# Optimization experiments

Hardware: AMD Instinct MI355X
Metric: run time of the kernel (lower is better)

Reference implementation:

```python
import jax, jax.numpy as jnp
import numpy as np

HUGE = 1e9  # stand-in for ops.HUGE_INT


def setup_inputs() -> dict:
    key = jax.random.key(0)
    ks = jax.random.split(key, 8)
    B, Q, K = 8, 128, 256
    Dq = Dk = Dv = H = 512
    query = jax.random.normal(ks[0], (B, Q, Dq), dtype=jnp.float32)
    k_ = jax.random.normal(ks[1], (B, K, Dk), dtype=jnp.float32)
    value = jax.random.normal(ks[2], (B, K, Dv), dtype=jnp.float32)
    mask = jax.random.randint(ks[3], (B, K), 0, 2, dtype=jnp.int32)
    # FFN params: linear1 (Dq+Dk -> H, bias), linear2 (H -> 1, no bias)
    W1 = jax.random.normal(ks[4], (Dq + Dk, H), dtype=jnp.float32) * 0.05
    b1 = jax.random.normal(ks[5], (H,), dtype=jnp.float32) * 0.05
    w2 = jax.random.normal(ks[6], (H, 1), dtype=jnp.float32) * 0.05
    return {"query": query, "key": k_, "value": value, "mask": mask,
            "W1": W1, "b1": b1, "w2": w2}


def reference(query, key, value, mask, W1, b1, w2):
    # Additive (FFN) attention. Original tiles query/key into [B, Q*K, Dq+Dk]
    # and applies linear1; concat@W1 is separable, so we project q and k
    # separately and broadcast-add (same math, no tiled concat tensor).
    Dq = query.shape[-1]
    Wq, Wk = W1[:Dq], W1[Dq:]
    q_proj = jnp.einsum('bqd,dh->bqh', query, Wq)   # [B,Q,H]
    k_proj = jnp.einsum('bkd,dh->bkh', key, Wk)     # [B,K,H]
    hidden = jnp.tanh(q_proj[:, :, None, :] + k_proj[:, None, :, :] + b1)  # [B,Q,K,H]
    scores = jnp.einsum('bqkh,h->bqk', hidden, w2[:, 0])  # [B,Q,K]
    # padding mask fill BEFORE scaling, matching the original op order
    scores = jnp.where(mask[:, None, :] != 0, -HUGE, scores)
    scores = scores / jnp.sqrt(jnp.float32(key.shape[-1]))
    attn_weights = jax.nn.softmax(scores, axis=-1)
    attn_vec = jnp.einsum('bqk,bkv->bqv', attn_weights, value)  # dropout=0 at eval
    return attn_vec, attn_weights
```

## Files before the change

### kernel.cpp

```cpp
#include <hip/hip_runtime.h>
#include <hip/hip_bf16.h>

#define B_ 8
#define Q_ 128
#define K_ 256
#define D_ 512
#define TWOLOG2E 2.8853900817779268f
#define SCALE 0.044194173824159216f
#define L2E 1.4426950408889634f
#define MASKVAL (-44194173.824159216f)

typedef __attribute__((ext_vector_type(8))) short frag8;
typedef __attribute__((ext_vector_type(4))) float f32x4;

__device__ __forceinline__ float fexp2(float x) {
  float r;
  asm("v_exp_f32 %0, %1" : "=v"(r) : "v"(x));
  return r;
}
__device__ __forceinline__ float frcp(float x) {
  float r;
  asm("v_rcp_f32 %0, %1" : "=v"(r) : "v"(x));
  return r;
}
__device__ __forceinline__ unsigned f2bf_u(float x) {
  unsigned u = __float_as_uint(x);
  return (u + 0x7FFFu + ((u >> 16) & 1u)) >> 16;
}
__device__ __forceinline__ unsigned short f2bf(float x) {
  return (unsigned short)f2bf_u(x);
}
__device__ __forceinline__ unsigned packbf(float lo, float hi) {
  return f2bf_u(lo) | (f2bf_u(hi) << 16);
}

__global__ __launch_bounds__(256) void gemm_kernel(
    const float* __restrict__ query, const float* __restrict__ key,
    const float* __restrict__ W1, const float* __restrict__ b1,
    float* __restrict__ qp, float* __restrict__ kpbT) {
  __shared__ short As[32 * 64];
  __shared__ short Bs[64 * 72];
  const int t = threadIdx.x;
  const int m0 = blockIdx.y * 32;
  const int n0 = blockIdx.x * 64;
  const bool is_k = (m0 >= B_ * Q_);
  const float* X = is_k ? key : query;
  const int xrow0 = is_k ? (m0 - B_ * Q_) : m0;
  const float* Wb = W1 + (is_k ? (size_t)D_ * D_ : 0);

  const int am = t >> 3;
  const int ac = t & 7;
  const float* gA = X + (size_t)(xrow0 + am) * D_ + ac * 8;
  short* aw = As + am * 64 + ((ac ^ (am & 7)) * 8);

  const int prow = t >> 4;
  const int n4 = (t & 15) * 4;
  const float* gB = Wb + n0 + n4;

  const int l = t & 63;
  const int w = t >> 6;
  const int lr = l & 15;
  const int kg = l >> 4;
  const int key8 = lr & 7;
  int aoff[2][2], boff[2];
#pragma unroll
  for (int kk = 0; kk < 2; ++kk) {
    const int cposA = ((kg + kk * 4) ^ key8) * 8;
#pragma unroll
    for (int mt = 0; mt < 2; ++mt) aoff[mt][kk] = (mt * 16 + lr) * 64 + cposA;
    boff[kk] = (w * 16 + lr) * 72 + (kg + kk * 4) * 8;
  }

  f32x4 acc[2];
  acc[0] = (f32x4){0.f, 0.f, 0.f, 0.f};
  acc[1] = (f32x4){0.f, 0.f, 0.f, 0.f};

  for (int k0 = 0; k0 < D_; k0 += 64) {
    float4 a0 = *(const float4*)(gA + k0);
    float4 a1 = *(const float4*)(gA + k0 + 4);
    float4 w00 = *(const float4*)(gB + (size_t)(k0 + 2 * prow) * D_);
    float4 w01 = *(const float4*)(gB + (size_t)(k0 + 2 * prow + 1) * D_);
    float4 w10 = *(const float4*)(gB + (size_t)(k0 + 2 * prow + 32) * D_);
    float4 w11 = *(const float4*)(gB + (size_t)(k0 + 2 * prow + 33) * D_);
    __syncthreads();
    {
      union { frag8 f; unsigned short u[8]; } av;
      av.u[0] = f2bf(a0.x); av.u[1] = f2bf(a0.y); av.u[2] = f2bf(a0.z); av.u[3] = f2bf(a0.w);
      av.u[4] = f2bf(a1.x); av.u[5] = f2bf(a1.y); av.u[6] = f2bf(a1.z); av.u[7] = f2bf(a1.w);
      *(frag8*)aw = av.f;
    }
    {
      float lo0[4] = {w00.x, w00.y, w00.z, w00.w};
      float hi0[4] = {w01.x, w01.y, w01.z, w01.w};
      float lo1[4] = {w10.x, w10.y, w10.z, w10.w};
      float hi1[4] = {w11.x, w11.y, w11.z, w11.w};
#pragma unroll
      for (int j = 0; j < 4; ++j) {
        *(unsigned*)(Bs + (n4 + j) * 72 + 2 * prow) = packbf(lo0[j], hi0[j]);
        *(unsigned*)(Bs + (n4 + j) * 72 + 2 * (prow + 16)) = packbf(lo1[j], hi1[j]);
      }
    }
    __syncthreads();
#pragma unroll
    for (int kk = 0; kk < 2; ++kk) {
      frag8 bf = *(const frag8*)(Bs + boff[kk]);
#pragma unroll
      for (int mt = 0; mt < 2; ++mt) {
        frag8 af = *(const frag8*)(As + aoff[mt][kk]);
        acc[mt] = __builtin_amdgcn_mfma_f32_16x16x32_bf16(af, bf, acc[mt], 0, 0, 0);
      }
    }
  }

  const int col = n0 + w * 16 + lr;
  if (is_k) {
    const float bc = b1[col];
#pragma unroll
    for (int mt = 0; mt < 2; ++mt) {
      const int krow = m0 - B_ * Q_ + mt * 16 + kg * 4;
      const int bb = krow >> 8;
      const int kk0 = krow & 255;
      float4 v;
      v.x = fexp2((acc[mt][0] + bc) * TWOLOG2E);
      v.y = fexp2((acc[mt][1] + bc) * TWOLOG2E);
      v.z = fexp2((acc[mt][2] + bc) * TWOLOG2E);
      v.w = fexp2((acc[mt][3] + bc) * TWOLOG2E);
      *(float4*)&kpbT[((size_t)bb * D_ + col) * K_ + kk0] = v;
    }
  } else {
#pragma unroll
    for (int mt = 0; mt < 2; ++mt) {
#pragma unroll
      for (int i = 0; i < 4; ++i) {
        const int row = m0 + mt * 16 + kg * 4 + i;
        qp[(size_t)row * D_ + col] = fexp2(acc[mt][i] * TWOLOG2E);
      }
    }
  }
}

__global__ __launch_bounds__(1024) void score_kernel(
    const float* __restrict__ qp, const float* __restrict__ kpbT,
    const int* __restrict__ mask, const float* __restrict__ w2,
    float* __restrict__ out_w) {
  __shared__ float smem_p[16 * 512];
  const int b = blockIdx.y;
  const int q0 = blockIdx.x * 4;
  const int t = threadIdx.x;
  const int lane = t & 63;
  const int w = __builtin_amdgcn_readfirstlane(t >> 6);
  const int kc = w & 1;
  const int hq = w >> 1;
  const int h0 = hq * 64;

  {
    const float* pk = kpbT + ((size_t)b * D_ + h0) * K_ + kc * 128 + 2 * lane;
    const float* q_0 = qp + (size_t)(b * Q_ + q0 + 0) * D_ + h0;
    const float* q_1 = qp + (size_t)(b * Q_ + q0 + 1) * D_ + h0;
    const float* q_2 = qp + (size_t)(b * Q_ + q0 + 2) * D_ + h0;
    const float* q_3 = qp + (size_t)(b * Q_ + q0 + 3) * D_ + h0;
    const float* w2h = w2 + h0;

    float2 a0 = {0.f, 0.f}, a1 = {0.f, 0.f}, a2 = {0.f, 0.f}, a3 = {0.f, 0.f};
    for (int h = 0; h < 64; h += 8) {
      float2 kv[8];
#pragma unroll
      for (int j = 0; j < 8; ++j) kv[j] = *(const float2*)&pk[(size_t)(h + j) * K_];
      float4 e0a = *(const float4*)(q_0 + h), e0b = *(const float4*)(q_0 + h + 4);
      float4 e1a = *(const float4*)(q_1 + h), e1b = *(const float4*)(q_1 + h + 4);
      float4 e2a = *(const float4*)(q_2 + h), e2b = *(const float4*)(q_2 + h + 4);
      float4 e3a = *(const float4*)(q_3 + h), e3b = *(const float4*)(q_3 + h + 4);
      float4 wa = *(const float4*)(w2h + h), wb = *(const float4*)(w2h + h + 4);
      float E0[8] = {e0a.x, e0a.y, e0a.z, e0a.w, e0b.x, e0b.y, e0b.z, e0b.w};
      float E1[8] = {e1a.x, e1a.y, e1a.z, e1a.w, e1b.x, e1b.y, e1b.z, e1b.w};
      float E2[8] = {e2a.x, e2a.y, e2a.z, e2a.w, e2b.x, e2b.y, e2b.z, e2b.w};
      float E3[8] = {e3a.x, e3a.y, e3a.z, e3a.w, e3b.x, e3b.y, e3b.z, e3b.w};
      float WV[8] = {wa.x, wa.y, wa.z, wa.w, wb.x, wb.y, wb.z, wb.w};
#pragma unroll
      for (int j = 0; j < 8; ++j) {
        a0.x = fmaf(WV[j], frcp(fmaf(E0[j], kv[j].x, 1.f)), a0.x);
        a0.y = fmaf(WV[j], frcp(fmaf(E0[j], kv[j].y, 1.f)), a0.y);
        a1.x = fmaf(WV[j], frcp(fmaf(E1[j], kv[j].x, 1.f)), a1.x);
        a1.y = fmaf(WV[j], frcp(fmaf(E1[j], kv[j].y, 1.f)), a1.y);
        a2.x = fmaf(WV[j], frcp(fmaf(E2[j], kv[j].x, 1.f)), a2.x);
        a2.y = fmaf(WV[j], frcp(fmaf(E2[j], kv[j].y, 1.f)), a2.y);
        a3.x = fmaf(WV[j], frcp(fmaf(E3[j], kv[j].x, 1.f)), a3.x);
        a3.y = fmaf(WV[j], frcp(fmaf(E3[j], kv[j].y, 1.f)), a3.y);
      }
    }
    *(float2*)&smem_p[w * 512 + 0 * 128 + 2 * lane] = a0;
    *(float2*)&smem_p[w * 512 + 1 * 128 + 2 * lane] = a1;
    *(float2*)&smem_p[w * 512 + 2 * 128 + 2 * lane] = a2;
    *(float2*)&smem_p[w * 512 + 3 * 128 + 2 * lane] = a3;
  }
  __syncthreads();

  if (w < 4) {
    const int q = w;
    float sw = 0.f;
#pragma unroll
    for (int m = 0; m < 8; ++m) sw += w2[lane + 64 * m];
#pragma unroll
    for (int off = 32; off; off >>= 1) sw += __shfl_xor(sw, off);

    float s[4];
#pragma unroll
    for (int r = 0; r < 4; ++r) {
      const int kcc = r >> 1;
      const int off = (r & 1) * 64 + lane;
      float p = 0.f;
#pragma unroll
      for (int hh = 0; hh < 8; ++hh)
        p += smem_p[(hh * 2 + kcc) * 512 + q * 128 + off];
      const int mk = mask[b * K_ + r * 64 + lane];
      s[r] = mk ? MASKVAL : fmaf(-2.f, p, sw) * SCALE;
    }
    float mx = fmaxf(fmaxf(s[0], s[1]), fmaxf(s[2], s[3]));
#pragma unroll
    for (int off = 32; off; off >>= 1) mx = fmaxf(mx, __shfl_xor(mx, off));
    float e[4], sum = 0.f;
#pragma unroll
    for (int r = 0; r < 4; ++r) {
      e[r] = fexp2((s[r] - mx) * L2E);
      sum += e[r];
    }
#pragma unroll
    for (int off = 32; off; off >>= 1) sum += __shfl_xor(sum, off);
    const float inv = frcp(sum);
    float* ow = out_w + (size_t)(b * Q_ + q0 + q) * K_;
#pragma unroll
    for (int r = 0; r < 4; ++r) ow[r * 64 + lane] = e[r] * inv;
  }
}

__global__ __launch_bounds__(1024) void pv_kernel(
    const float* __restrict__ out_w, const float* __restrict__ value,
    float* __restrict__ out_vec) {
  const int b = blockIdx.y;
  const int qt = blockIdx.x >> 3;
  const int ct = blockIdx.x & 7;
  const int t = threadIdx.x;
  const int lane = t & 63;
  const int w = __builtin_amdgcn_readfirstlane(t >> 6);
  const int col = ct * 64 + lane;
  const int q0 = qt * 32 + w * 2;

  const float* pw0 = out_w + (size_t)(b * Q_ + q0) * K_;
  const float* pw1 = pw0 + K_;
  const float* vb = value + (size_t)b * K_ * D_ + col;

  float o0 = 0.f, o1 = 0.f;
  for (int k = 0; k < K_; k += 4) {
    const float4 p0 = *(const float4*)&pw0[k];
    const float4 p1 = *(const float4*)&pw1[k];
    const float v0 = vb[(size_t)(k + 0) * D_];
    const float v1 = vb[(size_t)(k + 1) * D_];
    const float v2 = vb[(size_t)(k + 2) * D_];
    const float v3 = vb[(size_t)(k + 3) * D_];
    o0 = fmaf(p0.x, v0, fmaf(p0.y, v1, fmaf(p0.z, v2, fmaf(p0.w, v3, o0))));
    o1 = fmaf(p1.x, v0, fmaf(p1.y, v1, fmaf(p1.z, v2, fmaf(p1.w, v3, o1))));
  }
  out_vec[(size_t)(b * Q_ + q0) * D_ + col] = o0;
  out_vec[(size_t)(b * Q_ + q0 + 1) * D_ + col] = o1;
}

extern "C" void kernel_launch(void* const* d_in, const int* in_sizes, int n_in,
                              void* d_out, int out_size, void* d_ws, size_t ws_size,
                              hipStream_t stream) {
  const float* query = (const float*)d_in[0];
  const float* key   = (const float*)d_in[1];
  const float* value = (const float*)d_in[2];
  const int*   mask  = (const int*)d_in[3];
  const float* W1    = (const float*)d_in[4];
  const float* b1    = (const float*)d_in[5];
  const float* w2    = (const float*)d_in[6];

  float* out_vec = (float*)d_out;
  float* out_w   = out_vec + (size_t)B_ * Q_ * D_;

  float* qp   = (float*)d_ws;
  float* kpbT = qp + (size_t)B_ * Q_ * D_;

  gemm_kernel<<<dim3(8, 96), 256, 0, stream>>>(query, key, W1, b1, qp, kpbT);
  score_kernel<<<dim3(Q_ / 4, B_), 1024, 0, stream>>>(qp, kpbT, mask, w2, out_w);
  pv_kernel<<<dim3(32, B_), 1024, 0, stream>>>(out_w, value, out_vec);
}
```

Before: 113.9 us.

## Split score kernel over key halves and move softmax into PV kernel

The score kernel now splits each query tile's keys across two blocks, doubling the grid, and has each wave reduce 32 hidden units instead of 64. It writes raw masked scores to a workspace buffer. The softmax moves into the PV kernel, which normalises 32 rows into shared memory before the weighted sum over values. Softmax is recomputed by all 8 column blocks, and an extra score buffer adds a global round trip.

```diff
diff --git a/kernel.cpp b/kernel.cpp
--- a/kernel.cpp
+++ b/kernel.cpp
@@ -142,19 +142,19 @@
 __global__ __launch_bounds__(1024) void score_kernel(
     const float* __restrict__ qp, const float* __restrict__ kpbT,
     const int* __restrict__ mask, const float* __restrict__ w2,
-    float* __restrict__ out_w) {
+    float* __restrict__ sc) {
   __shared__ float smem_p[16 * 512];
   const int b = blockIdx.y;
-  const int q0 = blockIdx.x * 4;
+  const int qt = blockIdx.x >> 1;
+  const int kh = blockIdx.x & 1;
+  const int q0 = qt * 4;
   const int t = threadIdx.x;
   const int lane = t & 63;
   const int w = __builtin_amdgcn_readfirstlane(t >> 6);
-  const int kc = w & 1;
-  const int hq = w >> 1;
-  const int h0 = hq * 64;
+  const int h0 = w * 32;
 
   {
-    const float* pk = kpbT + ((size_t)b * D_ + h0) * K_ + kc * 128 + 2 * lane;
+    const float* pk = kpbT + ((size_t)b * D_ + h0) * K_ + kh * 128 + 2 * lane;
     const float* q_0 = qp + (size_t)(b * Q_ + q0 + 0) * D_ + h0;
     const float* q_1 = qp + (size_t)(b * Q_ + q0 + 1) * D_ + h0;
     const float* q_2 = qp + (size_t)(b * Q_ + q0 + 2) * D_ + h0;
@@ -162,7 +162,7 @@
     const float* w2h = w2 + h0;
 
     float2 a0 = {0.f, 0.f}, a1 = {0.f, 0.f}, a2 = {0.f, 0.f}, a3 = {0.f, 0.f};
-    for (int h = 0; h < 64; h += 8) {
+    for (int h = 0; h < 32; h += 8) {
       float2 kv[8];
 #pragma unroll
       for (int j = 0; j < 8; ++j) kv[j] = *(const float2*)&pk[(size_t)(h + j) * K_];
@@ -203,50 +203,58 @@
 #pragma unroll
     for (int off = 32; off; off >>= 1) sw += __shfl_xor(sw, off);
 
-    float s[4];
-#pragma unroll
-    for (int r = 0; r < 4; ++r) {
-      const int kcc = r >> 1;
-      const int off = (r & 1) * 64 + lane;
+    float* srow = sc + (size_t)(b * Q_ + q0 + q) * K_ + kh * 128;
+#pragma unroll
+    for (int half = 0; half < 2; ++half) {
+      const int pos = half * 64 + lane;
       float p = 0.f;
 #pragma unroll
-      for (int hh = 0; hh < 8; ++hh)
-        p += smem_p[(hh * 2 + kcc) * 512 + q * 128 + off];
-      const int mk = mask[b * K_ + r * 64 + lane];
-      s[r] = mk ? MASKVAL : fmaf(-2.f, p, sw) * SCALE;
-    }
-    float mx = fmaxf(fmaxf(s[0], s[1]), fmaxf(s[2], s[3]));
-#pragma unroll
-    for (int off = 32; off; off >>= 1) mx = fmaxf(mx, __shfl_xor(mx, off));
-    float e[4], sum = 0.f;
-#pragma unroll
-    for (int r = 0; r < 4; ++r) {
-      e[r] = fexp2((s[r] - mx) * L2E);
-      sum += e[r];
-    }
-#pragma unroll
-    for (int off = 32; off; off >>= 1) sum += __shfl_xor(sum, off);
-    const float inv = frcp(sum);
-    float* ow = out_w + (size_t)(b * Q_ + q0 + q) * K_;
-#pragma unroll
-    for (int r = 0; r < 4; ++r) ow[r * 64 + lane] = e[r] * inv;
+      for (int ww = 0; ww < 16; ++ww) p += smem_p[ww * 512 + q * 128 + pos];
+      const int mk = mask[b * K_ + kh * 128 + pos];
+      srow[pos] = mk ? MASKVAL : fmaf(-2.f, p, sw) * SCALE;
+    }
   }
 }
 
 __global__ __launch_bounds__(1024) void pv_kernel(
-    const float* __restrict__ out_w, const float* __restrict__ value,
-    float* __restrict__ out_vec) {
+    const float* __restrict__ sc, const float* __restrict__ value,
+    float* __restrict__ out_w, float* __restrict__ out_vec) {
+  __shared__ float pw[32 * 256];
   const int b = blockIdx.y;
   const int qt = blockIdx.x >> 3;
   const int ct = blockIdx.x & 7;
   const int t = threadIdx.x;
   const int lane = t & 63;
   const int w = __builtin_amdgcn_readfirstlane(t >> 6);
+
+#pragma unroll
+  for (int rr = 0; rr < 2; ++rr) {
+    const int row = w * 2 + rr;
+    const int q = qt * 32 + row;
+    const float* srow = sc + (size_t)(b * Q_ + q) * K_;
+    float4 sv = *(const float4*)&srow[lane * 4];
+    float mx = fmaxf(fmaxf(sv.x, sv.y), fmaxf(sv.z, sv.w));
+#pragma unroll
+    for (int off = 32; off; off >>= 1) mx = fmaxf(mx, __shfl_xor(mx, off));
+    float4 e;
+    e.x = fexp2((sv.x - mx) * L2E);
+    e.y = fexp2((sv.y - mx) * L2E);
+    e.z = fexp2((sv.z - mx) * L2E);
+    e.w = fexp2((sv.w - mx) * L2E);
+    float sum = e.x + e.y + e.z + e.w;
+#pragma unroll
+    for (int off = 32; off; off >>= 1) sum += __shfl_xor(sum, off);
+    const float inv = frcp(sum);
+    float4 p;
+    p.x = e.x * inv; p.y = e.y * inv; p.z = e.z * inv; p.w = e.w * inv;
+    *(float4*)&pw[row * 256 + lane * 4] = p;
+    if (ct == 0) *(float4*)&out_w[(size_t)(b * Q_ + q) * K_ + lane * 4] = p;
+  }
+  __syncthreads();
+
   const int col = ct * 64 + lane;
-  const int q0 = qt * 32 + w * 2;
-
-  const float* pw0 = out_w + (size_t)(b * Q_ + q0) * K_;
-  const float* pw1 = pw0 + K_;
+  const float* pw0 = &pw[(w * 2) * 256];
+  const float* pw1 = pw0 + 256;
   const float* vb = value + (size_t)b * K_ * D_ + col;
 
   float o0 = 0.f, o1 = 0.f;
@@ -260,8 +268,9 @@
     o0 = fmaf(p0.x, v0, fmaf(p0.y, v1, fmaf(p0.z, v2, fmaf(p0.w, v3, o0))));
     o1 = fmaf(p1.x, v0, fmaf(p1.y, v1, fmaf(p1.z, v2, fmaf(p1.w, v3, o1))));
   }
-  out_vec[(size_t)(b * Q_ + q0) * D_ + col] = o0;
-  out_vec[(size_t)(b * Q_ + q0 + 1) * D_ + col] = o1;
+  const int q0b = qt * 32 + w * 2;
+  out_vec[(size_t)(b * Q_ + q0b) * D_ + col] = o0;
+  out_vec[(size_t)(b * Q_ + q0b + 1) * D_ + col] = o1;
 }
 
 extern "C" void kernel_launch(void* const* d_in, const int* in_sizes, int n_in,
@@ -280,8 +289,9 @@
 
   float* qp   = (float*)d_ws;
   float* kpbT = qp + (size_t)B_ * Q_ * D_;
+  float* sc   = kpbT + (size_t)B_ * D_ * K_;
 
   gemm_kernel<<<dim3(8, 96), 256, 0, stream>>>(query, key, W1, b1, qp, kpbT);
-  score_kernel<<<dim3(Q_ / 4, B_), 1024, 0, stream>>>(qp, kpbT, mask, w2, out_w);
-  pv_kernel<<<dim3(32, B_), 1024, 0, stream>>>(out_w, value, out_vec);
-}
+  score_kernel<<<dim3(64, B_), 1024, 0, stream>>>(qp, kpbT, mask, w2, sc);
+  pv_kernel<<<dim3(32, B_), 1024, 0, stream>>>(sc, value, out_w, out_vec);
+}
```

After: 116.9 us. +2.6%, slower.
